# Performance work log

Hardware: AMD Instinct MI355X
Metric: run time of the kernel (lower is better)

The kernel has to match this reference:

```python
import jax, jax.numpy as jnp
import numpy as np

N, E, G = 50000, 800000, 1024      # nodes, edges, graphs
NF, R, H, O, B = 32, 4, 64, 16, 2  # node vocab, relations, hidden, output, conv blocks
MAX_DEG = 10                       # PyG MFConv default max_degree


def setup_inputs() -> dict:
    key = jax.random.key(0)
    ks = jax.random.split(key, 32)
    s = 0.05
    inp = {
        "x": jax.random.normal(ks[0], (N, NF), jnp.float32),
        "edge_attr": jax.random.normal(ks[1], (E, R), jnp.float32),
        "edge_index": jax.random.randint(ks[2], (2, E), 0, N),
        "batch_idx": jnp.sort(jax.random.randint(ks[3], (N,), 0, G)),
        "emb": jax.random.normal(ks[4], (NF, H), jnp.float32) * s,
        "lin1_w": jax.random.normal(ks[5], (H, H), jnp.float32) * s,
        "lin1_b": jnp.zeros((H,), jnp.float32),
        "lin2_w": jax.random.normal(ks[6], (H, O), jnp.float32) * s,
        "lin2_b": jnp.zeros((O,), jnp.float32),
    }
    for b in range(B):
        k = 7 + 4 * b
        inp[f"rgcn_w{b}"] = jax.random.normal(ks[k], (R, H, H), jnp.float32) * s
        inp[f"rgcn_root{b}"] = jax.random.normal(ks[k + 1], (H, H), jnp.float32) * s
        inp[f"rgcn_b{b}"] = jnp.zeros((H,), jnp.float32)
        inp[f"mf_wl{b}"] = jax.random.normal(ks[k + 2], (MAX_DEG + 1, H, H), jnp.float32) * s
        inp[f"mf_bl{b}"] = jnp.zeros((MAX_DEG + 1, H), jnp.float32)
        inp[f"mf_wr{b}"] = jax.random.normal(ks[k + 3], (MAX_DEG + 1, H, H), jnp.float32) * s
    return inp


def _rgcn(h, src, tgt, rel, W, Wroot, bias):
    # PyG RGCNConv: per-relation linear transform + per-(node,relation) MEAN aggregation + root + bias.
    hx = jnp.einsum('nh,rho->rno', h, W)            # [R,N,H] transformed features per relation
    m = hx[rel, src]                                # [E,H] per-edge messages
    seg = tgt * R + rel                             # segment id per (target node, relation)
    cnt = jax.ops.segment_sum(jnp.ones((E,), h.dtype), seg, num_segments=N * R)
    inv = jnp.where(cnt > 0, 1.0 / cnt, 0.0)
    agg = jax.ops.segment_sum(m * inv[seg][:, None], tgt, num_segments=N)
    return agg + h @ Wroot + bias


def _mfconv(h, src, tgt, Wl, bl, Wr):
    # PyG MFConv: sum-aggregate neighbors, then degree-indexed linear layers (lin_l has bias, lin_r none).
    deg = jnp.clip(jax.ops.segment_sum(jnp.ones((E,), jnp.int32), tgt, num_segments=N), 0, MAX_DEG)
    agg = jax.ops.segment_sum(h[src], tgt, num_segments=N)   # [N,H]
    out = jnp.zeros_like(h)
    for d in range(MAX_DEG + 1):                    # fixed small set of degree buckets
        mask = (deg == d)[:, None]
        out = out + jnp.where(mask, agg @ Wl[d] + bl[d] + h @ Wr[d], 0.0)
    return out


def reference(x, edge_index, edge_attr, batch_idx, emb,
              rgcn_w0, rgcn_root0, rgcn_b0, mf_wl0, mf_bl0, mf_wr0,
              rgcn_w1, rgcn_root1, rgcn_b1, mf_wl1, mf_bl1, mf_wr1,
              lin1_w, lin1_b, lin2_w, lin2_b):
    src, tgt = edge_index[0], edge_index[1]
    rel = jnp.argmax(edge_attr, axis=-1)
    h = emb[jnp.argmax(x, axis=-1)]                 # node embedding lookup
    blocks = [(rgcn_w0, rgcn_root0, rgcn_b0, mf_wl0, mf_bl0, mf_wr0),
              (rgcn_w1, rgcn_root1, rgcn_b1, mf_wl1, mf_bl1, mf_wr1)]
    for (W, Wro, bi, Wl, bl, Wr) in blocks:
        h = jax.nn.relu(h)
        h = _rgcn(h, src, tgt, rel, W, Wro, bi)
        h = jax.nn.relu(h)
        h = _mfconv(h, src, tgt, Wl, bl, Wr)
    g = jax.ops.segment_sum(h, batch_idx, num_segments=G)   # global add pool
    g = jax.nn.relu(g @ lin1_w + lin1_b)
    return g @ lin2_w + lin2_b
```

## Files before the change

kernel.cpp:

```cpp
#include <hip/hip_runtime.h>
#include <hip/hip_fp16.h>
#include <cstdint>
#include <cstddef>

#define Nn 50000
#define Ne 800000
#define Ng 1024
#define NFd 32
#define Rr 4
#define Hd 64
#define Od 16
#define MAXD 10
#define NSEG (Nn * Rr)
#define SCAN_BLK ((NSEG + 255) / 256)
#define ORDER_SZ (Nn + 176)
#define NB_MF (ORDER_SZ / 16)
#define NB_RG (Nn / 16)
#define NB_RELSEG (Ne / 256)
#define NB_EMBED (Nn / 8)
#define WT_PER_LAYER (Hd * 5 * Hd)
#define MFWT_PER_LAYER ((MAXD + 1) * Hd * 2 * Hd)
#define PREP_TOTAL (2 * WT_PER_LAYER + 2 * MFWT_PER_LAYER)

typedef _Float16 f16x8 __attribute__((ext_vector_type(8)));
typedef float f32x4 __attribute__((ext_vector_type(4)));

__device__ __forceinline__ float reluf(float v) { return v > 0.f ? v : 0.f; }
__device__ __forceinline__ int rfl(int v) { return __builtin_amdgcn_readfirstlane(v); }

__global__ void k_rel_emb(const float4* __restrict__ ea, const int* __restrict__ eidx,
                          int* __restrict__ seg, int* __restrict__ rank,
                          int* __restrict__ cnt,
                          const float* __restrict__ x, const float* __restrict__ emb,
                          __half* __restrict__ h16) {
    if (blockIdx.x < NB_RELSEG) {
        int e = blockIdx.x * 256 + threadIdx.x;
        float4 a = ea[e];
        int bi = 0; float bv = a.x;
        if (a.y > bv) { bv = a.y; bi = 1; }
        if (a.z > bv) { bv = a.z; bi = 2; }
        if (a.w > bv) { bv = a.w; bi = 3; }
        int s = eidx[Ne + e] * Rr + bi;
        seg[e] = s;
        rank[e] = atomicAdd(&cnt[s], 1);
    } else {
        int wave = ((blockIdx.x - NB_RELSEG) * 256 + threadIdx.x) >> 6;
        int lane = threadIdx.x & 63;
        int h = lane >> 5, q = lane & 31;
        int node = wave * 2 + h;
        float v = x[(size_t)node * NFd + q];
        int idx = q;
        #pragma unroll
        for (int o = 16; o >= 1; o >>= 1) {
            float ov = __shfl_xor(v, o);
            int oi = __shfl_xor(idx, o);
            if (ov > v || (ov == v && oi < idx)) { v = ov; idx = oi; }
        }
        const float2* e2 = (const float2*)(emb + (size_t)idx * Hd);
        float2 ev = e2[q];
        ((__half2*)h16)[(size_t)node * 32 + q] =
            __floats2half2_rn(reluf(ev.x), reluf(ev.y));
    }
}

__global__ void k_prep(const float* __restrict__ w0, const float* __restrict__ r0,
                       const float* __restrict__ w1, const float* __restrict__ r1,
                       const float* __restrict__ wl0, const float* __restrict__ wr0,
                       const float* __restrict__ wl1, const float* __restrict__ wr1,
                       __half* __restrict__ wt, __half* __restrict__ mfwt) {
    int idx = blockIdx.x * 256 + threadIdx.x;
    if (idx < 2 * WT_PER_LAYER) {
        int b = idx / WT_PER_LAYER;
        int rem = idx % WT_PER_LAYER;
        int c = rem / 320;
        int k = rem % 320;
        const float* W  = b ? w1 : w0;
        const float* Rt = b ? r1 : r0;
        float v = (k < 64) ? Rt[k * Hd + c]
                           : W[((size_t)((k - 64) >> 6)) * Hd * Hd + ((k - 64) & 63) * Hd + c];
        wt[idx] = __float2half(v);
    } else if (idx < PREP_TOTAL) {
        int j = idx - 2 * WT_PER_LAYER;
        int b = j / MFWT_PER_LAYER;
        int rem = j % MFWT_PER_LAYER;
        int d = rem / (Hd * 128);
        int r2 = rem % (Hd * 128);
        int c = r2 / 128;
        int k = r2 % 128;
        const float* Wl = b ? wl1 : wl0;
        const float* Wr = b ? wr1 : wr0;
        float v = (k < 64) ? Wl[(size_t)d * Hd * Hd + k * Hd + c]
                           : Wr[(size_t)d * Hd * Hd + (k - 64) * Hd + c];
        mfwt[j] = __float2half(v);
    }
}

__global__ void k_scan1(const int* __restrict__ cnt, int* __restrict__ off,
                        int* __restrict__ bsum, int* __restrict__ bcnt) {
    __shared__ int s[256];
    __shared__ int hist[16];
    int t = threadIdx.x;
    if (t < 16) hist[t] = 0;
    int idx = blockIdx.x * 256 + t;
    int v = (idx < NSEG) ? cnt[idx] : 0;
    s[t] = v;
    __syncthreads();
    if ((t & 3) == 0 && idx < NSEG) {
        int dsum = s[t] + s[t + 1] + s[t + 2] + s[t + 3];
        atomicAdd(&hist[min(dsum, MAXD)], 1);
    }
    #pragma unroll
    for (int o = 1; o < 256; o <<= 1) {
        int x = (t >= o) ? s[t - o] : 0;
        __syncthreads();
        s[t] += x;
        __syncthreads();
    }
    if (idx < NSEG) off[idx] = s[t] - v;
    if (t == 255) bsum[blockIdx.x] = s[255];
    if (t < 16) {
        int h = hist[t];
        if (h > 0) atomicAdd(&bcnt[t], h);
    }
}

__global__ void k_scan2(int* __restrict__ bsum, const int* __restrict__ bcnt,
                        int* __restrict__ bbase, int* __restrict__ order) {
    __shared__ int s[1024];
    int t = threadIdx.x;
    int v = (t < SCAN_BLK) ? bsum[t] : 0;
    s[t] = v;
    __syncthreads();
    #pragma unroll
    for (int o = 1; o < 1024; o <<= 1) {
        int x = (t >= o) ? s[t - o] : 0;
        __syncthreads();
        s[t] += x;
        __syncthreads();
    }
    if (t < SCAN_BLK) bsum[t] = s[t] - v;
    if (t == 0) {
        int run = 0;
        for (int d = 0; d <= MAXD; d++) {
            int c = bcnt[d];
            bbase[d] = run;
            int pad = (c + 15) & ~15;
            for (int i = c; i < pad; i++) order[run + i] = -1;
            run += pad;
        }
        for (int i = run; i < ORDER_SZ; i++) order[i] = -1;
    }
}

__global__ void k_scan3_bucket(int* __restrict__ off, const int* __restrict__ bsum,
                               const int4* __restrict__ cnt4, const int* __restrict__ bbase,
                               int* __restrict__ bfill, int* __restrict__ order) {
    __shared__ int hist[16];
    __shared__ int base[16];
    int t = threadIdx.x;
    if (t < 16) hist[t] = 0;
    __syncthreads();
    int idx = blockIdx.x * 256 + t;
    if (idx == 0) off[NSEG] = Ne;
    if (idx < NSEG) off[idx] = off[idx] + bsum[blockIdx.x];
    int d = 0, rk = 0;
    bool valid = (idx < Nn);
    if (valid) {
        int4 c = cnt4[idx];
        d = min(c.x + c.y + c.z + c.w, MAXD);
        rk = atomicAdd(&hist[d], 1);
    }
    __syncthreads();
    if (t < 16) {
        int h = hist[t];
        base[t] = (h > 0) ? atomicAdd(&bfill[t], h) : 0;
    }
    __syncthreads();
    if (valid) order[bbase[d] + base[d] + rk] = idx | (d << 20);
}

__global__ void k_scatter(const int* __restrict__ eidx, const int* __restrict__ seg,
                          const int* __restrict__ rank, const int* __restrict__ off,
                          int* __restrict__ sorted_src) {
    int e = blockIdx.x * 256 + threadIdx.x;
    if (e >= Ne) return;
    int pos = off[seg[e]] + rank[e];
    sorted_src[pos] = eidx[e];
}

__global__ __launch_bounds__(256) void k_rgcn_fused(
        const __half* __restrict__ hin16,
        const int* __restrict__ off, const int* __restrict__ ssrc,
        const __half* __restrict__ wt, const float* __restrict__ bias,
        __half* __restrict__ hout16) {
    __shared__ __align__(16) __half alds[16 * 296];
    int tid = threadIdx.x;
    int wv = tid >> 6, lane = tid & 63;
    int h = lane >> 5, q = lane & 31;
    int nblk = rfl(blockIdx.x * 16);
    int n0 = nblk + wv * 4;
    int obv = off[4 * n0 + min(lane, 16)];
    int cntv = __shfl(obv, lane + 1) - obv;
    float ivv = (cntv > 0) ? 1.f / (float)cntv : 0.f;
    int e    = rfl(__shfl(obv, 0));
    int eEnd = rfl(__shfl(obv, 16));
    const __half2* hp = (const __half2*)hin16;

    float ax = 0.f, ay = 0.f;
    float px = 0.f, py = 0.f;
    float vx = 0.f, vy = 0.f;
    int segi = 0;
    int nb = rfl(__shfl(obv, 1));

#define EMIT(SUB) do {                                               \
        float dx = ax - px, dy = ay - py;                            \
        float ox = ((SUB) && h) ? vx : 0.f;                          \
        float oy = ((SUB) && h) ? vy : 0.f;                          \
        dx -= ox; dy -= oy;                                          \
        dx += __shfl_xor(dx, 32); dy += __shfl_xor(dy, 32);          \
        float iv_ = __shfl(ivv, segi);                               \
        if (lane < 32)                                               \
            *(__half2*)&alds[(wv * 4 + (segi >> 2)) * 296            \
                             + (segi & 3) * 72 + 2 * q]              \
                = __floats2half2_rn(dx * iv_, dy * iv_);             \
        px = ax - ox; py = ay - oy;                                  \
        segi++;                                                      \
        nb = (segi < 16) ? rfl(__shfl(obv, segi + 1)) : 0x7fffffff;  \
    } while (0)

#define PSTEP(dj, t0) {                                              \
        while ((t0) == nb) EMIT(0);                                  \
        float2 f_ = __half22float2(dj);                              \
        vx = f_.x; vy = f_.y; ax += f_.x; ay += f_.y;                \
        while ((t0) + 1 == nb) EMIT(1); }

    if (e + 16 <= eEnd) {
        int4 iA = *(const int4*)(ssrc + e);
        int4 iB = *(const int4*)(ssrc + e + 4);
        int4 iC = *(const int4*)(ssrc + e + 8);
        int4 iD = *(const int4*)(ssrc + e + 12);
        while (true) {
            int s0 = h ? iA.y : iA.x;
            int s1 = h ? iA.w : iA.z;
            int s2 = h ? iB.y : iB.x;
            int s3 = h ? iB.w : iB.z;
            int s4 = h ? iC.y : iC.x;
            int s5 = h ? iC.w : iC.z;
            int s6 = h ? iD.y : iD.x;
            int s7 = h ? iD.w : iD.z;
            __half2 d0 = hp[s0 * 32 + q];
            __half2 d1 = hp[s1 * 32 + q];
            __half2 d2 = hp[s2 * 32 + q];
            __half2 d3 = hp[s3 * 32 + q];
            __half2 d4 = hp[s4 * 32 + q];
            __half2 d5 = hp[s5 * 32 + q];
            __half2 d6 = hp[s6 * 32 + q];
            __half2 d7 = hp[s7 * 32 + q];
            int en = e + 16;
            bool more = (en + 16 <= eEnd);
            int4 jA, jB, jC, jD;
            if (more) {
                jA = *(const int4*)(ssrc + en);
                jB = *(const int4*)(ssrc + en + 4);
                jC = *(const int4*)(ssrc + en + 8);
                jD = *(const int4*)(ssrc + en + 12);
            }
            PSTEP(d0, e + 0)  PSTEP(d1, e + 2)  PSTEP(d2, e + 4)  PSTEP(d3, e + 6)
            PSTEP(d4, e + 8)  PSTEP(d5, e + 10) PSTEP(d6, e + 12) PSTEP(d7, e + 14)
            e = en;
            if (!more) break;
            iA = jA; iB = jB; iC = jC; iD = jD;
        }
    }
    for (; e + 2 <= eEnd; e += 2) {
        while (e == nb) EMIT(0);
        int sa = rfl(ssrc[e]), sb = rfl(ssrc[e + 1]);
        int s = h ? sb : sa;
        float2 f = __half22float2(hp[s * 32 + q]);
        vx = f.x; vy = f.y; ax += f.x; ay += f.y;
        while (e + 1 == nb) EMIT(1);
    }
    if (e < eEnd) {
        while (e == nb) EMIT(0);
        int sa = rfl(ssrc[e]);
        float2 f = __half22float2(hp[sa * 32 + q]);
        if (h) { f.x = 0.f; f.y = 0.f; }
        ax += f.x; ay += f.y;
        e++;
    }
    while (segi < 16) EMIT(0);
#undef PSTEP
#undef EMIT

    __syncthreads();

    int rp = lane & 15;
    int g  = lane >> 4;
    const __half* ha = hin16 + (size_t)(nblk + rp) * Hd + 8 * g;
    const __half* ba = wt + (size_t)(wv * 16 + rp) * 320 + 8 * g;
    const __half* aa = alds + rp * 296 + 8 * g;
    f32x4 dacc = {0.f, 0.f, 0.f, 0.f};
    #pragma unroll
    for (int s = 0; s < 10; s++) {
        f16x8 bfrag = *(const f16x8*)(ba + s * 32);
        f16x8 afrag;
        if (s < 2) afrag = *(const f16x8*)(ha + s * 32);
        else       afrag = *(const f16x8*)(aa + ((s - 2) >> 1) * 72 + ((s - 2) & 1) * 32);
        dacc = __builtin_amdgcn_mfma_f32_16x16x32_f16(afrag, bfrag, dacc, 0, 0, 0);
    }
    int c = wv * 16 + rp;
    float bb = bias[c];
    #pragma unroll
    for (int j = 0; j < 4; j++) {
        int row = nblk + g * 4 + j;
        float v = reluf(dacc[j] + bb);
        hout16[(size_t)row * Hd + c] = __float2half(v);
    }
}

__global__ __launch_bounds__(256) void k_mf_fused(
        const __half* __restrict__ hin16,
        const int* __restrict__ off, const int* __restrict__ ssrc,
        const int* __restrict__ order, const __half* __restrict__ mfwt,
        const float* __restrict__ bl,
        float* __restrict__ hout, __half* __restrict__ hout16, int relu_out) {
    __shared__ __align__(16) __half alds[16 * 72];
    int tid = threadIdx.x;
    int wv = tid >> 6, lane = tid & 63;
    int g2 = lane >> 4, q4 = lane & 15;
    int blk = rfl(blockIdx.x * 16);
    int ent0 = rfl(order[blk]);
    if (ent0 < 0) return;
    int d = ent0 >> 20;
    const uint2* hp2 = (const uint2*)hin16;

#define SEL4(v4) ((g2 & 2) ? ((g2 & 1) ? (v4).w : (v4).z) : ((g2 & 1) ? (v4).y : (v4).x))
#define ACC8(dw) { float2 f_ = __half22float2(*(__half2*)&(dw).x);   \
                   float2 g_ = __half22float2(*(__half2*)&(dw).y);   \
                   a0 += f_.x; a1 += f_.y; a2 += g_.x; a3 += g_.y; }

    for (int i = 0; i < 4; i++) {
        int slot = blk + wv * 4 + i;
        int ent = rfl(order[slot]);
        float a0 = 0.f, a1 = 0.f, a2 = 0.f, a3 = 0.f;
        if (ent >= 0) {
            int n = ent & 0xFFFFF;
            int e0 = rfl(off[n * Rr]);
            int e4 = rfl(off[n * Rr + Rr]);
            int e = e0;
            for (; e + 16 <= e4; e += 16) {
                int4 iA = *(const int4*)(ssrc + e);
                int4 iB = *(const int4*)(ssrc + e + 4);
                int4 iC = *(const int4*)(ssrc + e + 8);
                int4 iD = *(const int4*)(ssrc + e + 12);
                int sA = SEL4(iA), sB = SEL4(iB), sC = SEL4(iC), sD = SEL4(iD);
                uint2 dA = hp2[(size_t)sA * 16 + q4];
                uint2 dB = hp2[(size_t)sB * 16 + q4];
                uint2 dC = hp2[(size_t)sC * 16 + q4];
                uint2 dD = hp2[(size_t)sD * 16 + q4];
                ACC8(dA) ACC8(dB) ACC8(dC) ACC8(dD)
            }
            for (; e + 4 <= e4; e += 4) {
                int4 iA = *(const int4*)(ssrc + e);
                int sA = SEL4(iA);
                uint2 dA = hp2[(size_t)sA * 16 + q4];
                ACC8(dA)
            }
            int rem = e4 - e;
            if (rem > 0) {
                int idxe = e + g2;
                int sl = ssrc[(idxe < e4) ? idxe : (e4 - 1)];
                uint2 dA = hp2[(size_t)sl * 16 + q4];
                float2 f = __half22float2(*(__half2*)&dA.x);
                float2 g = __half22float2(*(__half2*)&dA.y);
                if (idxe >= e4) { f.x = 0.f; f.y = 0.f; g.x = 0.f; g.y = 0.f; }
                a0 += f.x; a1 += f.y; a2 += g.x; a3 += g.y;
            }
        }
        a0 += __shfl_xor(a0, 16); a0 += __shfl_xor(a0, 32);
        a1 += __shfl_xor(a1, 16); a1 += __shfl_xor(a1, 32);
        a2 += __shfl_xor(a2, 16); a2 += __shfl_xor(a2, 32);
        a3 += __shfl_xor(a3, 16); a3 += __shfl_xor(a3, 32);
        if (lane < 16) {
            __half2* dst = (__half2*)&alds[(wv * 4 + i) * 72 + 4 * q4];
            dst[0] = __floats2half2_rn(a0, a1);
            dst[1] = __floats2half2_rn(a2, a3);
        }
    }
#undef SEL4
#undef ACC8
    __syncthreads();

    int rp = lane & 15;
    int g  = lane >> 4;
    int entr = order[blk + rp];
    int nr = (entr >= 0) ? (entr & 0xFFFFF) : 0;
    const __half* aa = alds + rp * 72 + 8 * g;
    const __half* ha = hin16 + (size_t)nr * Hd + 8 * g;
    const __half* ba = mfwt + ((size_t)d * Hd + wv * 16 + rp) * 128 + 8 * g;
    f32x4 dacc = {0.f, 0.f, 0.f, 0.f};
    #pragma unroll
    for (int s = 0; s < 4; s++) {
        f16x8 bfrag = *(const f16x8*)(ba + s * 32);
        f16x8 afrag = (s < 2) ? *(const f16x8*)(aa + s * 32)
                              : *(const f16x8*)(ha + (s - 2) * 32);
        dacc = __builtin_amdgcn_mfma_f32_16x16x32_f16(afrag, bfrag, dacc, 0, 0, 0);
    }
    int c = wv * 16 + rp;
    float bb = bl[d * Hd + c];
    #pragma unroll
    for (int j = 0; j < 4; j++) {
        int entw = order[blk + g * 4 + j];
        if (entw >= 0) {
            int n = entw & 0xFFFFF;
            float v = dacc[j] + bb;
            if (relu_out) hout16[(size_t)n * Hd + c] = __float2half(reluf(v));
            else          hout[(size_t)n * Hd + c] = v;
        }
    }
}

__global__ void k_pool(const float* __restrict__ h, const int* __restrict__ batch,
                       float* __restrict__ g) {
    int wave = rfl((blockIdx.x * 256 + threadIdx.x) >> 6);
    int lane = threadIdx.x & 63;
    int n0 = wave * 4;
    if (n0 >= Nn) return;
    int b0 = batch[n0], b1 = batch[n0 + 1], b2 = batch[n0 + 2], b3 = batch[n0 + 3];
    float v0 = h[(size_t)n0 * Hd + lane];
    float v1 = h[(size_t)(n0 + 1) * Hd + lane];
    float v2 = h[(size_t)(n0 + 2) * Hd + lane];
    float v3 = h[(size_t)(n0 + 3) * Hd + lane];
    if (b0 == b1 && b0 == b2 && b0 == b3) {
        unsafeAtomicAdd(&g[(size_t)b0 * Hd + lane], v0 + v1 + v2 + v3);
    } else {
        unsafeAtomicAdd(&g[(size_t)b0 * Hd + lane], v0);
        unsafeAtomicAdd(&g[(size_t)b1 * Hd + lane], v1);
        unsafeAtomicAdd(&g[(size_t)b2 * Hd + lane], v2);
        unsafeAtomicAdd(&g[(size_t)b3 * Hd + lane], v3);
    }
}

__global__ void k_head(const float* __restrict__ g, const float* __restrict__ w1,
                       const float* __restrict__ b1, const float* __restrict__ w2,
                       const float* __restrict__ b2, float* __restrict__ out) {
    __shared__ float t[4][Hd];
    int wv = threadIdx.x >> 6;
    int lane = threadIdx.x & 63;
    int gi = blockIdx.x * 4 + wv;
    float acc = b1[lane];
    for (int k = 0; k < Hd; k++) acc += g[(size_t)gi * Hd + k] * w1[k * Hd + lane];
    t[wv][lane] = reluf(acc);
    __syncthreads();
    if (lane < Od) {
        float o = b2[lane];
        for (int k = 0; k < Hd; k++) o += t[wv][k] * w2[k * Od + lane];
        out[(size_t)gi * Od + lane] = o;
    }
}

extern "C" void kernel_launch(void* const* d_in, const int* in_sizes, int n_in,
                              void* d_out, int out_size, void* d_ws, size_t ws_size,
                              hipStream_t stream) {
    const float* x      = (const float*)d_in[0];
    const float* ea     = (const float*)d_in[1];
    const int*   eidx   = (const int*)d_in[2];
    const int*   batch  = (const int*)d_in[3];
    const float* emb    = (const float*)d_in[4];
    const float* lin1_w = (const float*)d_in[5];
    const float* lin1_b = (const float*)d_in[6];
    const float* lin2_w = (const float*)d_in[7];
    const float* lin2_b = (const float*)d_in[8];
    const float* rgcn_w[2]    = {(const float*)d_in[9],  (const float*)d_in[15]};
    const float* rgcn_root[2] = {(const float*)d_in[10], (const float*)d_in[16]};
    const float* rgcn_b[2]    = {(const float*)d_in[11], (const float*)d_in[17]};
    const float* mf_wl[2]     = {(const float*)d_in[12], (const float*)d_in[18]};
    const float* mf_bl[2]     = {(const float*)d_in[13], (const float*)d_in[19]};
    const float* mf_wr[2]     = {(const float*)d_in[14], (const float*)d_in[20]};

    char* p = (char*)d_ws;
    float* h32   = (float*)p; p += sizeof(float) * (size_t)Nn * Hd;
    __half* h16a = (__half*)p; p += sizeof(__half) * (size_t)Nn * Hd;
    __half* h16b = (__half*)p; p += sizeof(__half) * (size_t)Nn * Hd;
    float* gbuf  = (float*)p; p += sizeof(float) * (size_t)Ng * Hd;
    __half* wt16 = (__half*)p; p += sizeof(__half) * (size_t)2 * WT_PER_LAYER;
    __half* mfwt16 = (__half*)p; p += sizeof(__half) * (size_t)2 * MFWT_PER_LAYER;
    int* seg     = (int*)p;   p += sizeof(int) * (size_t)Ne;
    int* rank    = (int*)p;   p += sizeof(int) * (size_t)Ne;
    int* ssrc    = (int*)p;   p += sizeof(int) * (size_t)Ne;
    int* cnt     = (int*)p;   p += sizeof(int) * (size_t)NSEG;
    int* bcnt    = (int*)p;   p += sizeof(int) * 16;
    int* bfill   = (int*)p;   p += sizeof(int) * 16;
    int* off     = (int*)p;   p += sizeof(int) * (size_t)(NSEG + 1);
    int* bsum    = (int*)p;   p += sizeof(int) * 1024;
    int* bbase   = (int*)p;   p += sizeof(int) * 16;
    int* order   = (int*)p;   p += sizeof(int) * (size_t)ORDER_SZ;

    hipMemsetAsync(cnt, 0, sizeof(int) * ((size_t)NSEG + 32), stream);
    hipMemsetAsync(gbuf, 0, sizeof(float) * (size_t)Ng * Hd, stream);

    k_prep<<<(PREP_TOTAL + 255) / 256, 256, 0, stream>>>(
        rgcn_w[0], rgcn_root[0], rgcn_w[1], rgcn_root[1],
        mf_wl[0], mf_wr[0], mf_wl[1], mf_wr[1], wt16, mfwt16);
    k_rel_emb<<<NB_RELSEG + NB_EMBED, 256, 0, stream>>>((const float4*)ea, eidx, seg, rank,
                                                        cnt, x, emb, h16a);
    k_scan1<<<SCAN_BLK, 256, 0, stream>>>(cnt, off, bsum, bcnt);
    k_scan2<<<1, 1024, 0, stream>>>(bsum, bcnt, bbase, order);
    k_scan3_bucket<<<SCAN_BLK, 256, 0, stream>>>(off, bsum, (const int4*)cnt, bbase,
                                                 bfill, order);
    k_scatter<<<Ne / 256, 256, 0, stream>>>(eidx, seg, rank, off, ssrc);

    __half* hin16 = h16a;  __half* hout16 = h16b;
    for (int b = 0; b < 2; b++) {
        k_rgcn_fused<<<NB_RG, 256, 0, stream>>>(hin16, off, ssrc, wt16 + b * WT_PER_LAYER,
                                                rgcn_b[b], hout16);
        k_mf_fused<<<NB_MF, 256, 0, stream>>>(hout16, off, ssrc, order,
                                              mfwt16 + b * MFWT_PER_LAYER, mf_bl[b],
                                              h32, hin16, b == 0 ? 1 : 0);
    }
    k_pool<<<Nn / 16, 256, 0, stream>>>(h32, batch, gbuf);
    k_head<<<Ng / 4, 256, 0, stream>>>(gbuf, lin1_w, lin1_b, lin2_w, lin2_b, (float*)d_out);
}
```

Measured before the change: 331.7 us.

## Fuse weight prep into embed kernel, pooling into MFConv, interleave neighbor gathers

Merges the weight-conversion kernel into the relation/embedding kernel as extra blocks and removes the separate pooling kernel. The final MFConv layer now atomically adds its outputs straight into the per-graph buffer, so the fp32 node feature array is no longer written. The MFConv neighbor aggregation processes four nodes per wave at the same time, with software-prefetched index loads, to expose more memory-level parallelism. In exchange there are many more scattered float atomics into the pooled buffer, more register pressure from the interleaved loop, and a different floating-point summation order.

```diff
diff --git a/kernel.cpp b/kernel.cpp
--- a/kernel.cpp
+++ b/kernel.cpp
@@ -21,6 +21,7 @@
 #define WT_PER_LAYER (Hd * 5 * Hd)
 #define MFWT_PER_LAYER ((MAXD + 1) * Hd * 2 * Hd)
 #define PREP_TOTAL (2 * WT_PER_LAYER + 2 * MFWT_PER_LAYER)
+#define NB_PREP ((PREP_TOTAL + 255) / 256)
 
 typedef _Float16 f16x8 __attribute__((ext_vector_type(8)));
 typedef float f32x4 __attribute__((ext_vector_type(4)));
@@ -32,7 +33,12 @@
                           int* __restrict__ seg, int* __restrict__ rank,
                           int* __restrict__ cnt,
                           const float* __restrict__ x, const float* __restrict__ emb,
-                          __half* __restrict__ h16) {
+                          __half* __restrict__ h16,
+                          const float* __restrict__ w0, const float* __restrict__ r0,
+                          const float* __restrict__ w1, const float* __restrict__ r1,
+                          const float* __restrict__ wl0, const float* __restrict__ wr0,
+                          const float* __restrict__ wl1, const float* __restrict__ wr1,
+                          __half* __restrict__ wt, __half* __restrict__ mfwt) {
     if (blockIdx.x < NB_RELSEG) {
         int e = blockIdx.x * 256 + threadIdx.x;
         float4 a = ea[e];
@@ -43,7 +49,7 @@
         int s = eidx[Ne + e] * Rr + bi;
         seg[e] = s;
         rank[e] = atomicAdd(&cnt[s], 1);
-    } else {
+    } else if (blockIdx.x < NB_RELSEG + NB_EMBED) {
         int wave = ((blockIdx.x - NB_RELSEG) * 256 + threadIdx.x) >> 6;
         int lane = threadIdx.x & 63;
         int h = lane >> 5, q = lane & 31;
@@ -60,38 +66,32 @@
         float2 ev = e2[q];
         ((__half2*)h16)[(size_t)node * 32 + q] =
             __floats2half2_rn(reluf(ev.x), reluf(ev.y));
-    }
-}
-
-__global__ void k_prep(const float* __restrict__ w0, const float* __restrict__ r0,
-                       const float* __restrict__ w1, const float* __restrict__ r1,
-                       const float* __restrict__ wl0, const float* __restrict__ wr0,
-                       const float* __restrict__ wl1, const float* __restrict__ wr1,
-                       __half* __restrict__ wt, __half* __restrict__ mfwt) {
-    int idx = blockIdx.x * 256 + threadIdx.x;
-    if (idx < 2 * WT_PER_LAYER) {
-        int b = idx / WT_PER_LAYER;
-        int rem = idx % WT_PER_LAYER;
-        int c = rem / 320;
-        int k = rem % 320;
-        const float* W  = b ? w1 : w0;
-        const float* Rt = b ? r1 : r0;
-        float v = (k < 64) ? Rt[k * Hd + c]
-                           : W[((size_t)((k - 64) >> 6)) * Hd * Hd + ((k - 64) & 63) * Hd + c];
-        wt[idx] = __float2half(v);
-    } else if (idx < PREP_TOTAL) {
-        int j = idx - 2 * WT_PER_LAYER;
-        int b = j / MFWT_PER_LAYER;
-        int rem = j % MFWT_PER_LAYER;
-        int d = rem / (Hd * 128);
-        int r2 = rem % (Hd * 128);
-        int c = r2 / 128;
-        int k = r2 % 128;
-        const float* Wl = b ? wl1 : wl0;
-        const float* Wr = b ? wr1 : wr0;
-        float v = (k < 64) ? Wl[(size_t)d * Hd * Hd + k * Hd + c]
-                           : Wr[(size_t)d * Hd * Hd + (k - 64) * Hd + c];
-        mfwt[j] = __float2half(v);
+    } else {
+        int idx = (blockIdx.x - NB_RELSEG - NB_EMBED) * 256 + threadIdx.x;
+        if (idx < 2 * WT_PER_LAYER) {
+            int b = idx / WT_PER_LAYER;
+            int rem = idx % WT_PER_LAYER;
+            int c = rem / 320;
+            int k = rem % 320;
+            const float* W  = b ? w1 : w0;
+            const float* Rt = b ? r1 : r0;
+            float v = (k < 64) ? Rt[k * Hd + c]
+                               : W[((size_t)((k - 64) >> 6)) * Hd * Hd + ((k - 64) & 63) * Hd + c];
+            wt[idx] = __float2half(v);
+        } else if (idx < PREP_TOTAL) {
+            int j = idx - 2 * WT_PER_LAYER;
+            int b = j / MFWT_PER_LAYER;
+            int rem = j % MFWT_PER_LAYER;
+            int d = rem / (Hd * 128);
+            int r2 = rem % (Hd * 128);
+            int c = r2 / 128;
+            int k = r2 % 128;
+            const float* Wl = b ? wl1 : wl0;
+            const float* Wr = b ? wr1 : wr0;
+            float v = (k < 64) ? Wl[(size_t)d * Hd * Hd + k * Hd + c]
+                               : Wr[(size_t)d * Hd * Hd + (k - 64) * Hd + c];
+            mfwt[j] = __float2half(v);
+        }
     }
 }
 
@@ -322,8 +322,8 @@
         const __half* __restrict__ hin16,
         const int* __restrict__ off, const int* __restrict__ ssrc,
         const int* __restrict__ order, const __half* __restrict__ mfwt,
-        const float* __restrict__ bl,
-        float* __restrict__ hout, __half* __restrict__ hout16, int relu_out) {
+        const float* __restrict__ bl, const int* __restrict__ batch,
+        float* __restrict__ gout, __half* __restrict__ hout16, int relu_out) {
     __shared__ __align__(16) __half alds[16 * 72];
     int tid = threadIdx.x;
     int wv = tid >> 6, lane = tid & 63;
@@ -335,60 +335,85 @@
     const uint2* hp2 = (const uint2*)hin16;
 
 #define SEL4(v4) ((g2 & 2) ? ((g2 & 1) ? (v4).w : (v4).z) : ((g2 & 1) ? (v4).y : (v4).x))
-#define ACC8(dw) { float2 f_ = __half22float2(*(__half2*)&(dw).x);   \
-                   float2 g_ = __half22float2(*(__half2*)&(dw).y);   \
-                   a0 += f_.x; a1 += f_.y; a2 += g_.x; a3 += g_.y; }
-
-    for (int i = 0; i < 4; i++) {
-        int slot = blk + wv * 4 + i;
-        int ent = rfl(order[slot]);
-        float a0 = 0.f, a1 = 0.f, a2 = 0.f, a3 = 0.f;
-        if (ent >= 0) {
-            int n = ent & 0xFFFFF;
-            int e0 = rfl(off[n * Rr]);
-            int e4 = rfl(off[n * Rr + Rr]);
-            int e = e0;
-            for (; e + 16 <= e4; e += 16) {
-                int4 iA = *(const int4*)(ssrc + e);
-                int4 iB = *(const int4*)(ssrc + e + 4);
-                int4 iC = *(const int4*)(ssrc + e + 8);
-                int4 iD = *(const int4*)(ssrc + e + 12);
-                int sA = SEL4(iA), sB = SEL4(iB), sC = SEL4(iC), sD = SEL4(iD);
-                uint2 dA = hp2[(size_t)sA * 16 + q4];
-                uint2 dB = hp2[(size_t)sB * 16 + q4];
-                uint2 dC = hp2[(size_t)sC * 16 + q4];
-                uint2 dD = hp2[(size_t)sD * 16 + q4];
-                ACC8(dA) ACC8(dB) ACC8(dC) ACC8(dD)
-            }
-            for (; e + 4 <= e4; e += 4) {
-                int4 iA = *(const int4*)(ssrc + e);
-                int sA = SEL4(iA);
-                uint2 dA = hp2[(size_t)sA * 16 + q4];
-                ACC8(dA)
-            }
-            int rem = e4 - e;
-            if (rem > 0) {
-                int idxe = e + g2;
-                int sl = ssrc[(idxe < e4) ? idxe : (e4 - 1)];
-                uint2 dA = hp2[(size_t)sl * 16 + q4];
-                float2 f = __half22float2(*(__half2*)&dA.x);
-                float2 g = __half22float2(*(__half2*)&dA.y);
-                if (idxe >= e4) { f.x = 0.f; f.y = 0.f; g.x = 0.f; g.y = 0.f; }
-                a0 += f.x; a1 += f.y; a2 += g.x; a3 += g.y;
-            }
-        }
-        a0 += __shfl_xor(a0, 16); a0 += __shfl_xor(a0, 32);
-        a1 += __shfl_xor(a1, 16); a1 += __shfl_xor(a1, 32);
-        a2 += __shfl_xor(a2, 16); a2 += __shfl_xor(a2, 32);
-        a3 += __shfl_xor(a3, 16); a3 += __shfl_xor(a3, 32);
-        if (lane < 16) {
-            __half2* dst = (__half2*)&alds[(wv * 4 + i) * 72 + 4 * q4];
-            dst[0] = __floats2half2_rn(a0, a1);
-            dst[1] = __floats2half2_rn(a2, a3);
-        }
-    }
+#define ACC8V(dw, P) { float2 f_ = __half22float2(*(__half2*)&(dw).x);  \
+                       float2 h_ = __half22float2(*(__half2*)&(dw).y);  \
+                       P.x += f_.x; P.y += f_.y; P.z += h_.x; P.w += h_.y; }
+#define TAILQ(ec, ee, P) if ((ec) < (ee)) {                             \
+        int idxe = (ec) + g2;                                           \
+        int sl = ssrc[(idxe < (ee)) ? idxe : ((ee) - 1)];               \
+        uint2 dw = hp2[(size_t)sl * 16 + q4];                           \
+        float2 f_ = __half22float2(*(__half2*)&dw.x);                   \
+        float2 h_ = __half22float2(*(__half2*)&dw.y);                   \
+        if (idxe >= (ee)) { f_.x = 0.f; f_.y = 0.f; h_.x = 0.f; h_.y = 0.f; } \
+        P.x += f_.x; P.y += f_.y; P.z += h_.x; P.w += h_.y; }
+#define REDW(P, i) {                                                    \
+        P.x += __shfl_xor(P.x, 16); P.x += __shfl_xor(P.x, 32);         \
+        P.y += __shfl_xor(P.y, 16); P.y += __shfl_xor(P.y, 32);         \
+        P.z += __shfl_xor(P.z, 16); P.z += __shfl_xor(P.z, 32);         \
+        P.w += __shfl_xor(P.w, 16); P.w += __shfl_xor(P.w, 32);         \
+        if (lane < 16) {                                                \
+            __half2* dst = (__half2*)&alds[(wv * 4 + (i)) * 72 + 4 * q4]; \
+            dst[0] = __floats2half2_rn(P.x, P.y);                       \
+            dst[1] = __floats2half2_rn(P.z, P.w); } }
+
+    int entA = rfl(order[blk + wv * 4 + 0]);
+    int entB = rfl(order[blk + wv * 4 + 1]);
+    int entC = rfl(order[blk + wv * 4 + 2]);
+    int entD = rfl(order[blk + wv * 4 + 3]);
+    int nA = (entA >= 0) ? (entA & 0xFFFFF) : 0;
+    int nB = (entB >= 0) ? (entB & 0xFFFFF) : 0;
+    int nC = (entC >= 0) ? (entC & 0xFFFFF) : 0;
+    int nD = (entD >= 0) ? (entD & 0xFFFFF) : 0;
+    int eA = rfl(off[nA * Rr]), endA = (entA >= 0) ? rfl(off[nA * Rr + Rr]) : eA;
+    int eB = rfl(off[nB * Rr]), endB = (entB >= 0) ? rfl(off[nB * Rr + Rr]) : eB;
+    int eC = rfl(off[nC * Rr]), endC = (entC >= 0) ? rfl(off[nC * Rr + Rr]) : eC;
+    int eD = rfl(off[nD * Rr]), endD = (entD >= 0) ? rfl(off[nD * Rr + Rr]) : eD;
+
+    float4 accA = {0.f, 0.f, 0.f, 0.f}, accB = {0.f, 0.f, 0.f, 0.f};
+    float4 accC = {0.f, 0.f, 0.f, 0.f}, accD = {0.f, 0.f, 0.f, 0.f};
+
+    bool aA = (eA + 4 <= endA), aB = (eB + 4 <= endB);
+    bool aC = (eC + 4 <= endC), aD = (eD + 4 <= endD);
+    int4 ixA, ixB, ixC, ixD;
+    if (aA) ixA = *(const int4*)(ssrc + eA);
+    if (aB) ixB = *(const int4*)(ssrc + eB);
+    if (aC) ixC = *(const int4*)(ssrc + eC);
+    if (aD) ixD = *(const int4*)(ssrc + eD);
+    while (aA | aB | aC | aD) {
+        uint2 dA, dB, dC, dD;
+        if (aA) { int s = SEL4(ixA); dA = hp2[(size_t)s * 16 + q4]; }
+        if (aB) { int s = SEL4(ixB); dB = hp2[(size_t)s * 16 + q4]; }
+        if (aC) { int s = SEL4(ixC); dC = hp2[(size_t)s * 16 + q4]; }
+        if (aD) { int s = SEL4(ixD); dD = hp2[(size_t)s * 16 + q4]; }
+        bool pA = false, pB = false, pC = false, pD = false;
+        if (aA) { eA += 4; pA = (eA + 4 <= endA); }
+        if (aB) { eB += 4; pB = (eB + 4 <= endB); }
+        if (aC) { eC += 4; pC = (eC + 4 <= endC); }
+        if (aD) { eD += 4; pD = (eD + 4 <= endD); }
+        int4 jxA, jxB, jxC, jxD;
+        if (pA) jxA = *(const int4*)(ssrc + eA);
+        if (pB) jxB = *(const int4*)(ssrc + eB);
+        if (pC) jxC = *(const int4*)(ssrc + eC);
+        if (pD) jxD = *(const int4*)(ssrc + eD);
+        if (aA) ACC8V(dA, accA)
+        if (aB) ACC8V(dB, accB)
+        if (aC) ACC8V(dC, accC)
+        if (aD) ACC8V(dD, accD)
+        if (pA) ixA = jxA;
+        if (pB) ixB = jxB;
+        if (pC) ixC = jxC;
+        if (pD) ixD = jxD;
+        aA = pA; aB = pB; aC = pC; aD = pD;
+    }
+    TAILQ(eA, endA, accA)
+    TAILQ(eB, endB, accB)
+    TAILQ(eC, endC, accC)
+    TAILQ(eD, endD, accD)
+    REDW(accA, 0) REDW(accB, 1) REDW(accC, 2) REDW(accD, 3)
 #undef SEL4
-#undef ACC8
+#undef ACC8V
+#undef TAILQ
+#undef REDW
     __syncthreads();
 
     int rp = lane & 15;
@@ -415,29 +440,8 @@
             int n = entw & 0xFFFFF;
             float v = dacc[j] + bb;
             if (relu_out) hout16[(size_t)n * Hd + c] = __float2half(reluf(v));
-            else          hout[(size_t)n * Hd + c] = v;
+            else unsafeAtomicAdd(&gout[(size_t)batch[n] * Hd + c], v);
         }
-    }
-}
-
-__global__ void k_pool(const float* __restrict__ h, const int* __restrict__ batch,
-                       float* __restrict__ g) {
-    int wave = rfl((blockIdx.x * 256 + threadIdx.x) >> 6);
-    int lane = threadIdx.x & 63;
-    int n0 = wave * 4;
-    if (n0 >= Nn) return;
-    int b0 = batch[n0], b1 = batch[n0 + 1], b2 = batch[n0 + 2], b3 = batch[n0 + 3];
-    float v0 = h[(size_t)n0 * Hd + lane];
-    float v1 = h[(size_t)(n0 + 1) * Hd + lane];
-    float v2 = h[(size_t)(n0 + 2) * Hd + lane];
-    float v3 = h[(size_t)(n0 + 3) * Hd + lane];
-    if (b0 == b1 && b0 == b2 && b0 == b3) {
-        unsafeAtomicAdd(&g[(size_t)b0 * Hd + lane], v0 + v1 + v2 + v3);
-    } else {
-        unsafeAtomicAdd(&g[(size_t)b0 * Hd + lane], v0);
-        unsafeAtomicAdd(&g[(size_t)b1 * Hd + lane], v1);
-        unsafeAtomicAdd(&g[(size_t)b2 * Hd + lane], v2);
-        unsafeAtomicAdd(&g[(size_t)b3 * Hd + lane], v3);
     }
 }
 
@@ -479,7 +483,6 @@
     const float* mf_wr[2]     = {(const float*)d_in[14], (const float*)d_in[20]};
 
     char* p = (char*)d_ws;
-    float* h32   = (float*)p; p += sizeof(float) * (size_t)Nn * Hd;
     __half* h16a = (__half*)p; p += sizeof(__half) * (size_t)Nn * Hd;
     __half* h16b = (__half*)p; p += sizeof(__half) * (size_t)Nn * Hd;
     float* gbuf  = (float*)p; p += sizeof(float) * (size_t)Ng * Hd;
@@ -499,11 +502,10 @@
     hipMemsetAsync(cnt, 0, sizeof(int) * ((size_t)NSEG + 32), stream);
     hipMemsetAsync(gbuf, 0, sizeof(float) * (size_t)Ng * Hd, stream);
 
-    k_prep<<<(PREP_TOTAL + 255) / 256, 256, 0, stream>>>(
+    k_rel_emb<<<NB_RELSEG + NB_EMBED + NB_PREP, 256, 0, stream>>>(
+        (const float4*)ea, eidx, seg, rank, cnt, x, emb, h16a,
         rgcn_w[0], rgcn_root[0], rgcn_w[1], rgcn_root[1],
         mf_wl[0], mf_wr[0], mf_wl[1], mf_wr[1], wt16, mfwt16);
-    k_rel_emb<<<NB_RELSEG + NB_EMBED, 256, 0, stream>>>((const float4*)ea, eidx, seg, rank,
-                                                        cnt, x, emb, h16a);
     k_scan1<<<SCAN_BLK, 256, 0, stream>>>(cnt, off, bsum, bcnt);
     k_scan2<<<1, 1024, 0, stream>>>(bsum, bcnt, bbase, order);
     k_scan3_bucket<<<SCAN_BLK, 256, 0, stream>>>(off, bsum, (const int4*)cnt, bbase,
@@ -516,8 +518,7 @@
                                                 rgcn_b[b], hout16);
         k_mf_fused<<<NB_MF, 256, 0, stream>>>(hout16, off, ssrc, order,
                                               mfwt16 + b * MFWT_PER_LAYER, mf_bl[b],
-                                              h32, hin16, b == 0 ? 1 : 0);
-    }
-    k_pool<<<Nn / 16, 256, 0, stream>>>(h32, batch, gbuf);
+                                              batch, gbuf, hin16, b == 0 ? 1 : 0);
+    }
     k_head<<<Ng / 4, 256, 0, stream>>>(gbuf, lin1_w, lin1_b, lin2_w, lin2_b, (float*)d_out);
 }
```

Result: slower. 365.1 us (+10.0%).
